# Performance work log

Measured on AMD Instinct MI355X. Metric: run time of the kernel, lower is better.

## Reference

```python
import jax, jax.numpy as jnp
import numpy as np
from jax import lax

B, T, H = 32768, 64, 16
VOCAB_USER = 600001
VOCAB_LAUNCH = 3


def setup_inputs() -> dict:
    key = jax.random.key(0)
    ks = jax.random.split(key, 10)
    s = 1.0 / np.sqrt(H)
    return {
        "user_id": jax.random.randint(ks[0], (B,), 0, VOCAB_USER),
        "launch_seq": jax.random.randint(ks[1], (B, T), 0, VOCAB_LAUNCH),
        "user_emb": jax.random.normal(ks[2], (VOCAB_USER, H), dtype=jnp.float32),
        "launch_emb": jax.random.normal(ks[3], (VOCAB_LAUNCH, H), dtype=jnp.float32),
        "W_ih": jax.random.uniform(ks[4], (3 * H, H), jnp.float32, -s, s),
        "W_hh": jax.random.uniform(ks[5], (3 * H, H), jnp.float32, -s, s),
        "b_ih": jax.random.uniform(ks[6], (3 * H,), jnp.float32, -s, s),
        "b_hh": jax.random.uniform(ks[7], (3 * H,), jnp.float32, -s, s),
        "fc_W": jax.random.uniform(ks[8], (1, 2 * H), jnp.float32, -s, s),
        "fc_b": jax.random.uniform(ks[9], (1,), jnp.float32, -s, s),
    }


def reference(user_id, launch_seq, user_emb, launch_emb, W_ih, W_hh, b_ih, b_hh, fc_W, fc_b):
    u = user_emb[user_id]                      # (B, H)
    x = launch_emb[launch_seq]                 # (B, T, H)
    # precompute input contributions to the gates for all timesteps
    gx_all = jnp.einsum('bth,gh->btg', x, W_ih) + b_ih  # (B, T, 3H)

    def step(h, gx):
        gh = h @ W_hh.T + b_hh                 # (B, 3H)
        r = jax.nn.sigmoid(gx[:, :H] + gh[:, :H])
        z = jax.nn.sigmoid(gx[:, H:2 * H] + gh[:, H:2 * H])
        n = jnp.tanh(gx[:, 2 * H:] + r * gh[:, 2 * H:])
        h_new = (1.0 - z) * n + z * h
        return h_new, h_new

    h0 = jnp.zeros((x.shape[0], H), dtype=x.dtype)
    _, hs = lax.scan(step, h0, jnp.swapaxes(gx_all, 0, 1))  # hs: (T, B, H)
    pooled = jnp.mean(hs, axis=0)              # (B, H)
    fc_in = jnp.concatenate([u, pooled], axis=1)  # (B, 2H)
    return fc_in @ fc_W.T + fc_b               # (B, 1)
```

## Files before the change

kernel.cpp:

```cpp
#include <hip/hip_runtime.h>
#include <hip/hip_bf16.h>
#include <string.h>


#define NBLK 2048

typedef __attribute__((ext_vector_type(8))) short short8;
typedef __attribute__((ext_vector_type(4))) float floatx4;

static __device__ __forceinline__ float fexp2(float x) { return __builtin_amdgcn_exp2f(x); }
static __device__ __forceinline__ float frcp(float x)  { return __builtin_amdgcn_rcpf(x); }

static __device__ __forceinline__ unsigned short bf16_bits(float f) {
    __hip_bfloat16 b = __float2bfloat16(f);
    union { __hip_bfloat16 b; unsigned short u; } cv; cv.b = b; return cv.u;
}
static __device__ __forceinline__ float bf16_f32(unsigned short u) {
    unsigned v = ((unsigned)u) << 16; float f; memcpy(&f, &v, 4); return f;
}

__global__ __launch_bounds__(64) void gru_mfma(
    const int* __restrict__ user_id,
    const int* __restrict__ launch_seq,
    const float* __restrict__ user_emb,
    const float* __restrict__ launch_emb,
    const float* __restrict__ W_ih,
    const float* __restrict__ W_hh,
    const float* __restrict__ b_ih,
    const float* __restrict__ b_hh,
    const float* __restrict__ fc_W,
    const float* __restrict__ fc_b,
    float* __restrict__ out)
{
    constexpr float L  = 1.4426950408889634f;
    constexpr float L2 = 2.8853900817779268f;

    __shared__ float gxr[48], gxz[48], gxn[48];
    __shared__ unsigned char  seqb[16 * 68];
    __shared__ unsigned short hhi[16 * 32];
    __shared__ unsigned short hlo[16 * 32];

    const int tid  = threadIdx.x;
    const int col  = tid & 15;
    const int quad = tid >> 4;
    const long long sampBase = (long long)blockIdx.x * 16;

    {
        int r = tid >> 2, w = tid & 3;
        const int* sp = launch_seq + (sampBase + r) * 64 + w * 16;
        #pragma unroll
        for (int g = 0; g < 4; ++g) {
            int4 v = ((const int4*)sp)[g];
            unsigned pk = (unsigned)v.x | ((unsigned)v.y << 8) |
                          ((unsigned)v.z << 16) | ((unsigned)v.w << 24);
            *(unsigned*)(seqb + r * 68 + w * 16 + g * 4) = pk;
        }
    }

    for (int idx = tid; idx < 144; idx += 64) {
        int s = idx / 48;
        int g = idx - s * 48;
        float dot = b_ih[g];
        #pragma unroll
        for (int k = 0; k < 16; ++k)
            dot = fmaf(W_ih[g * 16 + k], launch_emb[s * 16 + k], dot);
        int d = g & 15;
        if (g < 16)      gxr[s * 16 + d] = -L * (dot + b_hh[g]);
        else if (g < 32) gxz[s * 16 + d] = -L * (dot + b_hh[g]);
        else             gxn[s * 16 + d] =  L2 * dot;
    }

    for (int i = tid; i < 256; i += 64) {
        ((unsigned*)hhi)[i] = 0u;
        ((unsigned*)hlo)[i] = 0u;
    }

    short8 Brh, Brl, Bzh, Bzl, Bnh, Bnl;
    #pragma unroll
    for (int j = 0; j < 8; ++j) {
        int k = quad * 8 + j;
        float wr = 0.f, wz = 0.f, wn = 0.f;
        if (k < 16) {
            wr = -L  * W_hh[(col)      * 16 + k];
            wz = -L  * W_hh[(16 + col) * 16 + k];
            wn =  L2 * W_hh[(32 + col) * 16 + k];
        }
        unsigned short h;
        h = bf16_bits(wr); Brh[j] = (short)h; Brl[j] = (short)bf16_bits(wr - bf16_f32(h));
        h = bf16_bits(wz); Bzh[j] = (short)h; Bzl[j] = (short)bf16_bits(wz - bf16_f32(h));
        h = bf16_bits(wn); Bnh[j] = (short)h; Bnl[j] = (short)bf16_bits(wn - bf16_f32(h));
    }

    const float bhn = L2 * b_hh[32 + col];
    const floatx4 Cn_init = {bhn, bhn, bhn, bhn};

    const int a_off = col * 64 + (((quad + col + (col >> 2)) & 3) << 4);
    int w_off[4], seq_base[4];
    #pragma unroll
    for (int i = 0; i < 4; ++i) {
        int s = quad * 4 + i;
        w_off[i] = s * 64 + ((((col >> 3) + s + (s >> 2)) & 3) << 4) + (col & 7) * 2;
        seq_base[i] = s * 68;
    }

    floatx4 h    = {0.f, 0.f, 0.f, 0.f};
    floatx4 pool = {0.f, 0.f, 0.f, 0.f};
    short8 Ahi = {0, 0, 0, 0, 0, 0, 0, 0};
    short8 Alo = {0, 0, 0, 0, 0, 0, 0, 0};

    __syncthreads();

    #pragma unroll 4
    for (int t = 0; t < 64; ++t) {
        int s0 = seqb[seq_base[0] + t];
        int s1 = seqb[seq_base[1] + t];
        int s2 = seqb[seq_base[2] + t];
        int s3 = seqb[seq_base[3] + t];

        floatx4 accr, accz;
        accr.x = gxr[(s0 << 4) + col]; accr.y = gxr[(s1 << 4) + col];
        accr.z = gxr[(s2 << 4) + col]; accr.w = gxr[(s3 << 4) + col];
        accz.x = gxz[(s0 << 4) + col]; accz.y = gxz[(s1 << 4) + col];
        accz.z = gxz[(s2 << 4) + col]; accz.w = gxz[(s3 << 4) + col];
        float gn[4];
        gn[0] = gxn[(s0 << 4) + col]; gn[1] = gxn[(s1 << 4) + col];
        gn[2] = gxn[(s2 << 4) + col]; gn[3] = gxn[(s3 << 4) + col];

        accr = __builtin_amdgcn_mfma_f32_16x16x32_bf16(Ahi, Brh, accr, 0, 0, 0);
        accr = __builtin_amdgcn_mfma_f32_16x16x32_bf16(Alo, Brh, accr, 0, 0, 0);
        accr = __builtin_amdgcn_mfma_f32_16x16x32_bf16(Ahi, Brl, accr, 0, 0, 0);
        accz = __builtin_amdgcn_mfma_f32_16x16x32_bf16(Ahi, Bzh, accz, 0, 0, 0);
        accz = __builtin_amdgcn_mfma_f32_16x16x32_bf16(Alo, Bzh, accz, 0, 0, 0);
        accz = __builtin_amdgcn_mfma_f32_16x16x32_bf16(Ahi, Bzl, accz, 0, 0, 0);
        floatx4 accn;
        accn = __builtin_amdgcn_mfma_f32_16x16x32_bf16(Ahi, Bnh, Cn_init, 0, 0, 0);
        accn = __builtin_amdgcn_mfma_f32_16x16x32_bf16(Alo, Bnh, accn, 0, 0, 0);
        accn = __builtin_amdgcn_mfma_f32_16x16x32_bf16(Ahi, Bnl, accn, 0, 0, 0);

        #pragma unroll
        for (int i = 0; i < 4; ++i) {
            float r  = frcp(1.0f + fexp2(accr[i]));
            float z  = frcp(1.0f + fexp2(accz[i]));
            float y  = fmaf(r, accn[i], gn[i]);
            float n  = fmaf(-2.0f, frcp(1.0f + fexp2(y)), 1.0f);
            float hn = fmaf(z, h[i] - n, n);
            h[i] = hn;
            pool[i] += hn;
            unsigned short hb = bf16_bits(hn);
            *(unsigned short*)((char*)hhi + w_off[i]) = hb;
            *(unsigned short*)((char*)hlo + w_off[i]) = bf16_bits(hn - bf16_f32(hb));
        }

        __syncthreads();
        Ahi = *(const short8*)((const char*)hhi + a_off);
        Alo = *(const short8*)((const char*)hlo + a_off);
    }

    const float fw1 = fc_W[col];
    const float fw2 = fc_W[16 + col] * (1.0f / 64.0f);
    #pragma unroll
    for (int i = 0; i < 4; ++i) {
        int s = quad * 4 + i;
        int uid = user_id[sampBase + s];
        float u = user_emb[(long long)uid * 16 + col];
        float v = fmaf(u, fw1, pool[i] * fw2);
        v += __shfl_xor(v, 1);
        v += __shfl_xor(v, 2);
        v += __shfl_xor(v, 4);
        v += __shfl_xor(v, 8);
        if (col == 0) out[sampBase + s] = v + fc_b[0];
    }
}

extern "C" void kernel_launch(void* const* d_in, const int* in_sizes, int n_in,
                              void* d_out, int out_size, void* d_ws, size_t ws_size,
                              hipStream_t stream) {
    const int*   user_id    = (const int*)d_in[0];
    const int*   launch_seq = (const int*)d_in[1];
    const float* user_emb   = (const float*)d_in[2];
    const float* launch_emb = (const float*)d_in[3];
    const float* W_ih       = (const float*)d_in[4];
    const float* W_hh       = (const float*)d_in[5];
    const float* b_ih       = (const float*)d_in[6];
    const float* b_hh       = (const float*)d_in[7];
    const float* fc_W       = (const float*)d_in[8];
    const float* fc_b       = (const float*)d_in[9];
    float* out = (float*)d_out;

    gru_mfma<<<dim3(NBLK), dim3(64), 0, stream>>>(
        user_id, launch_seq, user_emb, launch_emb,
        W_ih, W_hh, b_ih, b_hh, fc_W, fc_b, out);
}
```

Before: 145.6 us.

## Remove per-step barrier via double-buffered packed hidden state and register gate LUT

Replaces the per-timestep __syncthreads with double-buffered LDS storage of the hidden state. Each hidden value's bf16 hi/lo pair is packed into one dword, and the MFMA A operands are rebuilt with perm instructions. The input-gate lookup table moves into registers, picked with selects by the 3-valued token id, and the sequence is transposed so one dword load per step serves four samples. MFMA issue order is interleaved across the r/z/n gates to add ILP. With a single-wave block the barrier is arguably unnecessary, but correctness now relies on wave-level LDS ordering, and the 3-entry select assumes the vocab of 3.

```diff
diff --git a/kernel.cpp b/kernel.cpp
--- a/kernel.cpp
+++ b/kernel.cpp
@@ -5,18 +5,19 @@
 
 #define NBLK 2048
 
-typedef __attribute__((ext_vector_type(8))) short short8;
-typedef __attribute__((ext_vector_type(4))) float floatx4;
+typedef __attribute__((ext_vector_type(8))) short   short8;
+typedef __attribute__((ext_vector_type(4))) float   floatx4;
+typedef __attribute__((ext_vector_type(4))) unsigned uintx4;
 
 static __device__ __forceinline__ float fexp2(float x) { return __builtin_amdgcn_exp2f(x); }
 static __device__ __forceinline__ float frcp(float x)  { return __builtin_amdgcn_rcpf(x); }
-
-static __device__ __forceinline__ unsigned short bf16_bits(float f) {
-    __hip_bfloat16 b = __float2bfloat16(f);
-    union { __hip_bfloat16 b; unsigned short u; } cv; cv.b = b; return cv.u;
+static __device__ __forceinline__ unsigned f2u(float f) { unsigned u; memcpy(&u, &f, 4); return u; }
+static __device__ __forceinline__ float u2f(unsigned u) { float f; memcpy(&f, &u, 4); return f; }
+static __device__ __forceinline__ unsigned short bf16_rne(float f) {
+    union { __hip_bfloat16 b; unsigned short u; } cv; cv.b = __float2bfloat16(f); return cv.u;
 }
-static __device__ __forceinline__ float bf16_f32(unsigned short u) {
-    unsigned v = ((unsigned)u) << 16; float f; memcpy(&f, &v, 4); return f;
+static __device__ __forceinline__ float sel3(int c, float a0, float a1, float a2) {
+    return c == 0 ? a0 : (c == 1 ? a1 : a2);
 }
 
 __global__ __launch_bounds__(64) void gru_mfma(
@@ -35,10 +36,9 @@
     constexpr float L  = 1.4426950408889634f;
     constexpr float L2 = 2.8853900817779268f;
 
-    __shared__ float gxr[48], gxz[48], gxn[48];
-    __shared__ unsigned char  seqb[16 * 68];
-    __shared__ unsigned short hhi[16 * 32];
-    __shared__ unsigned short hlo[16 * 32];
+    __shared__ float         gxlut[192];
+    __shared__ unsigned char seqT[1024];
+    __shared__ unsigned      hlds[512];
 
     const int tid  = threadIdx.x;
     const int col  = tid & 15;
@@ -51,28 +51,21 @@
         #pragma unroll
         for (int g = 0; g < 4; ++g) {
             int4 v = ((const int4*)sp)[g];
-            unsigned pk = (unsigned)v.x | ((unsigned)v.y << 8) |
-                          ((unsigned)v.z << 16) | ((unsigned)v.w << 24);
-            *(unsigned*)(seqb + r * 68 + w * 16 + g * 4) = pk;
+            int t0 = w * 16 + g * 4;
+            seqT[(t0 + 0) * 16 + r] = (unsigned char)v.x;
+            seqT[(t0 + 1) * 16 + r] = (unsigned char)v.y;
+            seqT[(t0 + 2) * 16 + r] = (unsigned char)v.z;
+            seqT[(t0 + 3) * 16 + r] = (unsigned char)v.w;
         }
     }
 
     for (int idx = tid; idx < 144; idx += 64) {
-        int s = idx / 48;
-        int g = idx - s * 48;
+        int s = idx / 48, g = idx - s * 48;
         float dot = b_ih[g];
         #pragma unroll
         for (int k = 0; k < 16; ++k)
             dot = fmaf(W_ih[g * 16 + k], launch_emb[s * 16 + k], dot);
-        int d = g & 15;
-        if (g < 16)      gxr[s * 16 + d] = -L * (dot + b_hh[g]);
-        else if (g < 32) gxz[s * 16 + d] = -L * (dot + b_hh[g]);
-        else             gxn[s * 16 + d] =  L2 * dot;
-    }
-
-    for (int i = tid; i < 256; i += 64) {
-        ((unsigned*)hhi)[i] = 0u;
-        ((unsigned*)hlo)[i] = 0u;
+        gxlut[g * 4 + s] = (g < 32) ? (-L * (dot + b_hh[g])) : (L2 * dot);
     }
 
     short8 Brh, Brl, Bzh, Bzl, Bnh, Bnl;
@@ -85,56 +78,60 @@
             wz = -L  * W_hh[(16 + col) * 16 + k];
             wn =  L2 * W_hh[(32 + col) * 16 + k];
         }
-        unsigned short h;
-        h = bf16_bits(wr); Brh[j] = (short)h; Brl[j] = (short)bf16_bits(wr - bf16_f32(h));
-        h = bf16_bits(wz); Bzh[j] = (short)h; Bzl[j] = (short)bf16_bits(wz - bf16_f32(h));
-        h = bf16_bits(wn); Bnh[j] = (short)h; Bnl[j] = (short)bf16_bits(wn - bf16_f32(h));
+        unsigned short hb;
+        hb = bf16_rne(wr); Brh[j] = (short)hb; Brl[j] = (short)bf16_rne(wr - u2f((unsigned)hb << 16));
+        hb = bf16_rne(wz); Bzh[j] = (short)hb; Bzl[j] = (short)bf16_rne(wz - u2f((unsigned)hb << 16));
+        hb = bf16_rne(wn); Bnh[j] = (short)hb; Bnl[j] = (short)bf16_rne(wn - u2f((unsigned)hb << 16));
     }
+    const float bhn = L2 * b_hh[32 + col];
+    const floatx4 CnInit = {bhn, bhn, bhn, bhn};
 
-    const float bhn = L2 * b_hh[32 + col];
-    const floatx4 Cn_init = {bhn, bhn, bhn, bhn};
+    __syncthreads();
 
-    const int a_off = col * 64 + (((quad + col + (col >> 2)) & 3) << 4);
-    int w_off[4], seq_base[4];
+    float4 vr = *(const float4*)&gxlut[(col)      * 4];
+    float4 vz = *(const float4*)&gxlut[(16 + col) * 4];
+    float4 vn = *(const float4*)&gxlut[(32 + col) * 4];
+
+    const int qa = quad & 1;
+    const int p0 = ((qa * 8) + 4 * ((col >> 1) & 3)) & 15;
+    const int a_dw1 = col * 16 + p0;
+    const int a_dw2 = col * 16 + ((p0 + 4) & 15);
+    int w_dw[4];
     #pragma unroll
     for (int i = 0; i < 4; ++i) {
         int s = quad * 4 + i;
-        w_off[i] = s * 64 + ((((col >> 3) + s + (s >> 2)) & 3) << 4) + (col & 7) * 2;
-        seq_base[i] = s * 68;
+        w_dw[i] = s * 16 + ((col + 4 * ((s >> 1) & 3)) & 15);
     }
 
     floatx4 h    = {0.f, 0.f, 0.f, 0.f};
     floatx4 pool = {0.f, 0.f, 0.f, 0.f};
     short8 Ahi = {0, 0, 0, 0, 0, 0, 0, 0};
     short8 Alo = {0, 0, 0, 0, 0, 0, 0, 0};
-
-    __syncthreads();
+    unsigned seq_dw = *(const unsigned*)&seqT[quad * 4];
 
     #pragma unroll 4
     for (int t = 0; t < 64; ++t) {
-        int s0 = seqb[seq_base[0] + t];
-        int s1 = seqb[seq_base[1] + t];
-        int s2 = seqb[seq_base[2] + t];
-        int s3 = seqb[seq_base[3] + t];
+        const int wb = (t & 1) ? 256 : 0;
 
-        floatx4 accr, accz;
-        accr.x = gxr[(s0 << 4) + col]; accr.y = gxr[(s1 << 4) + col];
-        accr.z = gxr[(s2 << 4) + col]; accr.w = gxr[(s3 << 4) + col];
-        accz.x = gxz[(s0 << 4) + col]; accz.y = gxz[(s1 << 4) + col];
-        accz.z = gxz[(s2 << 4) + col]; accz.w = gxz[(s3 << 4) + col];
-        float gn[4];
-        gn[0] = gxn[(s0 << 4) + col]; gn[1] = gxn[(s1 << 4) + col];
-        gn[2] = gxn[(s2 << 4) + col]; gn[3] = gxn[(s3 << 4) + col];
+        int c0 = seq_dw & 3, c1 = (seq_dw >> 8) & 3,
+            c2 = (seq_dw >> 16) & 3, c3 = (seq_dw >> 24) & 3;
+        floatx4 accr = { sel3(c0, vr.x, vr.y, vr.z), sel3(c1, vr.x, vr.y, vr.z),
+                         sel3(c2, vr.x, vr.y, vr.z), sel3(c3, vr.x, vr.y, vr.z) };
+        floatx4 accz = { sel3(c0, vz.x, vz.y, vz.z), sel3(c1, vz.x, vz.y, vz.z),
+                         sel3(c2, vz.x, vz.y, vz.z), sel3(c3, vz.x, vz.y, vz.z) };
+        float gn[4]  = { sel3(c0, vn.x, vn.y, vn.z), sel3(c1, vn.x, vn.y, vn.z),
+                         sel3(c2, vn.x, vn.y, vn.z), sel3(c3, vn.x, vn.y, vn.z) };
+
+        seq_dw = *(const unsigned*)&seqT[((t + 1) & 63) * 16 + quad * 4];
 
         accr = __builtin_amdgcn_mfma_f32_16x16x32_bf16(Ahi, Brh, accr, 0, 0, 0);
+        accz = __builtin_amdgcn_mfma_f32_16x16x32_bf16(Ahi, Bzh, accz, 0, 0, 0);
+        floatx4 accn = __builtin_amdgcn_mfma_f32_16x16x32_bf16(Ahi, Bnh, CnInit, 0, 0, 0);
         accr = __builtin_amdgcn_mfma_f32_16x16x32_bf16(Alo, Brh, accr, 0, 0, 0);
+        accz = __builtin_amdgcn_mfma_f32_16x16x32_bf16(Alo, Bzh, accz, 0, 0, 0);
+        accn = __builtin_amdgcn_mfma_f32_16x16x32_bf16(Alo, Bnh, accn, 0, 0, 0);
         accr = __builtin_amdgcn_mfma_f32_16x16x32_bf16(Ahi, Brl, accr, 0, 0, 0);
-        accz = __builtin_amdgcn_mfma_f32_16x16x32_bf16(Ahi, Bzh, accz, 0, 0, 0);
-        accz = __builtin_amdgcn_mfma_f32_16x16x32_bf16(Alo, Bzh, accz, 0, 0, 0);
         accz = __builtin_amdgcn_mfma_f32_16x16x32_bf16(Ahi, Bzl, accz, 0, 0, 0);
-        floatx4 accn;
-        accn = __builtin_amdgcn_mfma_f32_16x16x32_bf16(Ahi, Bnh, Cn_init, 0, 0, 0);
-        accn = __builtin_amdgcn_mfma_f32_16x16x32_bf16(Alo, Bnh, accn, 0, 0, 0);
         accn = __builtin_amdgcn_mfma_f32_16x16x32_bf16(Ahi, Bnl, accn, 0, 0, 0);
 
         #pragma unroll
@@ -146,14 +143,23 @@
             float hn = fmaf(z, h[i] - n, n);
             h[i] = hn;
             pool[i] += hn;
-            unsigned short hb = bf16_bits(hn);
-            *(unsigned short*)((char*)hhi + w_off[i]) = hb;
-            *(unsigned short*)((char*)hlo + w_off[i]) = bf16_bits(hn - bf16_f32(hb));
+            unsigned u  = f2u(hn);
+            float  lof  = hn - u2f(u & 0xffff0000u);
+            hlds[wb + w_dw[i]] = __builtin_amdgcn_perm(f2u(lof), u, 0x07060302u);
         }
 
-        __syncthreads();
-        Ahi = *(const short8*)((const char*)hhi + a_off);
-        Alo = *(const short8*)((const char*)hlo + a_off);
+        uintx4 A1 = *(const uintx4*)&hlds[wb + a_dw1];
+        uintx4 A2 = *(const uintx4*)&hlds[wb + a_dw2];
+        uintx4 hi4 = { __builtin_amdgcn_perm(A1.y, A1.x, 0x05040100u),
+                       __builtin_amdgcn_perm(A1.w, A1.z, 0x05040100u),
+                       __builtin_amdgcn_perm(A2.y, A2.x, 0x05040100u),
+                       __builtin_amdgcn_perm(A2.w, A2.z, 0x05040100u) };
+        uintx4 lo4 = { __builtin_amdgcn_perm(A1.y, A1.x, 0x07060302u),
+                       __builtin_amdgcn_perm(A1.w, A1.z, 0x07060302u),
+                       __builtin_amdgcn_perm(A2.y, A2.x, 0x07060302u),
+                       __builtin_amdgcn_perm(A2.w, A2.z, 0x07060302u) };
+        Ahi = __builtin_bit_cast(short8, hi4);
+        Alo = __builtin_bit_cast(short8, lo4);
     }
 
     const float fw1 = fc_W[col];
```

Measured after the change: 145.1 us. Within noise of the previous version (-0.3%).
